# Optimization experiments

Measured on AMD Instinct MI355X. Metric: run time of the kernel, lower is better.

## Reference

```python
import jax, jax.numpy as jnp
import numpy as np
from jax import lax

D = 128      # d_model
NH = 8       # nhead
DIM = D // NH
B, H, W = 2, 160, 160
EPS_ATT = 1e-6


def setup_inputs() -> dict:
    key = jax.random.key(0)
    ks = iter(jax.random.split(key, 40))
    def n(*s):
        return jax.random.normal(next(ks), s, dtype=jnp.float32) * 0.05
    inp = {
        "x": jax.random.normal(next(ks), (B, D, H, W), jnp.float32),
        "source": jax.random.normal(next(ks), (B, D, H, W), jnp.float32),
        # q/k/v 1x1 conv (with bias)
        "wq": n(D, D), "bq": n(D),
        "wk": n(D, D), "bk": n(D),
        "wv": n(D, D), "bv": n(D),
        # multiscale aggregation (scale=5): depthwise 5x5 (no bias) + pointwise 1x1 (no bias)
        "dwq": n(D, 1, 5, 5), "pwq": n(D, D),
        "dwk": n(D, 1, 5, 5), "pwk": n(D, D),
        "dwv": n(D, 1, 5, 5), "pwv": n(D, D),
        # attention output projection: 2*d_model -> d_model, no bias
        "wproj": n(D, 2 * D),
        # merge 1x1 conv
        "wmerge": n(D, D), "bmerge": n(D),
        # conv ffn: d -> 2d -> d
        "wff1": n(2 * D, D), "bff1": n(2 * D),
        "wff2": n(D, 2 * D), "bff2": n(D),
        # layernorms over channel dim
        "ln1_w": 1.0 + n(D), "ln1_b": n(D),
        "ln2_w": 1.0 + n(D), "ln2_b": n(D),
    }
    return inp


def _pw(t, Wm, b=None):
    # 1x1 conv as channel matmul; t: [B,C,H,W], Wm: [O,C]
    y = jnp.einsum('bchw,oc->bohw', t, Wm)
    return y if b is None else y + b[None, :, None, None]


def _bn(t):
    # BatchNorm2d, training-mode batch stats, affine=False, eps=1e-5
    m = t.mean((0, 2, 3), keepdims=True)
    v = t.var((0, 2, 3), keepdims=True)
    return (t - m) * lax.rsqrt(v + 1e-5)


def _gelu(t):
    return jax.nn.gelu(t, approximate=False)


def _dw(t, Wk):
    # depthwise 5x5 conv, stride 1, SAME padding (== padding=2)
    return lax.conv_general_dilated(t, Wk, (1, 1), 'SAME',
                                    dimension_numbers=('NCHW', 'OIHW', 'NCHW'),
                                    feature_group_count=D)


def _ln(t, w, b):
    # LayerNorm over channel axis of NCHW tensor, eps=1e-5
    m = t.mean(1, keepdims=True)
    v = t.var(1, keepdims=True)
    return (t - m) * lax.rsqrt(v + 1e-5) * w[None, :, None, None] + b[None, :, None, None]


def reference(x, source, wq, bq, wk, bk, wv, bv, dwq, pwq, dwk, pwk, dwv, pwv,
              wproj, wmerge, bmerge, wff1, bff1, wff2, bff2,
              ln1_w, ln1_b, ln2_w, ln2_b):
    q = _gelu(_bn(_pw(x, wq, bq)))
    k = _gelu(_bn(_pw(source, wk, bk)))
    v = _gelu(_bn(_pw(source, wv, bv)))

    # multiscale aggregation: concat original with one scale-5 depthwise+pointwise branch
    qc = jnp.concatenate([q, _pw(_dw(q, dwq), pwq)], axis=1)
    kc = jnp.concatenate([k, _pw(_dw(k, dwk), pwk)], axis=1)
    vc = jnp.concatenate([v, _pw(_dw(v, dwv), pwv)], axis=1)

    qc = jax.nn.relu(qc)  # kernel feature map
    kc = jax.nn.relu(kc)

    b_, C2, h1, w1 = qc.shape           # C2 = 2*d_model
    h2, w2 = kc.shape[2], kc.shape[3]
    L1, L2 = h1 * w1, h2 * w2
    H2 = C2 // DIM                       # effective heads = 2*nhead

    qf = qc.reshape(b_, C2, L1).transpose(0, 2, 1).reshape(b_, L1, H2, DIM)
    kf = kc.reshape(b_, C2, L2).transpose(0, 2, 1).reshape(b_, L2, H2, DIM)
    vf = vc.reshape(b_, C2, L2).transpose(0, 2, 1).reshape(b_, L2, H2, DIM)

    vf = vf / L2
    kv = jnp.einsum('nshd,nshv->nhdv', kf, vf)                       # [b,H2,d,d]
    z = 1.0 / jnp.maximum(jnp.einsum('nlhd,nhd->nlh', qf, kf.sum(1) / L2), EPS_ATT)
    qv = jnp.einsum('nlhd,nhdv,nlh->nlhv', qf, kv, z)                # [b,L1,H2,d]

    out = qv.transpose(0, 2, 3, 1).reshape(b_, C2, h1, w1)
    msg = _pw(out, wproj)                                            # 2d -> d

    msg = _gelu(_bn(_pw(msg, wmerge, bmerge)))
    msg = x + msg
    msg = _ln(msg, ln1_w, ln1_b)

    ff = _gelu(_bn(_pw(msg, wff1, bff1)))
    ff = _gelu(_bn(_pw(ff, wff2, bff2)))
    return _ln(ff + msg, ln2_w, ln2_b)
```

## Files before the change

kernel.cpp:

```cpp
#include <hip/hip_runtime.h>
#include <math.h>

#define LL 25600
#define NTOTF 51200.f
#define NSH 8

using f16   = _Float16;
using f16x8 = __attribute__((ext_vector_type(8))) _Float16;
using f16x4 = __attribute__((ext_vector_type(4))) _Float16;
using f16x2 = __attribute__((ext_vector_type(2))) _Float16;
using f32x4 = __attribute__((ext_vector_type(4))) float;

__device__ __forceinline__ float gelu_f(float v) {
    const float u2 = v * (1.5957691216057308f + 0.0713548162726009f * v * v);
    const float e  = __expf(u2);
    return v * (1.f - 1.f / (e + 1.f));
}

__device__ __forceinline__ void stat_mr(const float* st, int C, int c,
                                        float& m, float& r) {
    float s1 = 0.f, s2 = 0.f;
#pragma unroll
    for (int sh = 0; sh < NSH; ++sh) {
        s1 += st[sh * 2 * C + c];
        s2 += st[sh * 2 * C + C + c];
    }
    m = s1 * (1.f / NTOTF);
    r = rsqrtf(s2 * (1.f / NTOTF) - m * m + 1e-5f);
}

template <int M, int K, int PP, int NSEG, bool IN32, bool LDG, bool TWOW,
          bool BIAS, bool STATS>
__global__ __launch_bounds__(512, 2) void gemm_kernel(
    const void* __restrict__ X1, const void* __restrict__ X2,
    const void* __restrict__ X3,
    const float* __restrict__ WA, const float* __restrict__ WB,
    const float* __restrict__ W2, const float* __restrict__ W3,
    const float* __restrict__ biasA, const float* __restrict__ biasB,
    const float* __restrict__ lstat,
    f16* __restrict__ Y1, f16* __restrict__ Y2, f16* __restrict__ Y3,
    float* __restrict__ ostat)
{
    constexpr int MR  = M / 128;
    constexpr int KS  = K / 32;
    constexpr int NR  = PP / 16;
    constexpr int PG  = PP / 8;
    constexpr int NCH = (K * PG) / 512;
    constexpr int NCHUNK = LL / PP;

    __shared__ f16 Xs[PP * K];

    const int tid  = threadIdx.x;
    const int lane = tid & 63;
    const int wv   = tid >> 6;
    const int lm16 = lane & 15, lg = lane >> 4;
    const int row0 = wv * (M / 8);

    int bx = blockIdx.x, seg = 0;
    if (NSEG > 1) { seg = bx / (2 * NCHUNK); bx -= seg * 2 * NCHUNK; }
    const int bb  = bx / NCHUNK;
    const int pp0 = (bx - bb * NCHUNK) * PP;

    const void*  Xp = (NSEG > 1) ? (seg == 0 ? X1 : (seg == 1 ? X2 : X3)) : X1;
    const float* Wp = (NSEG > 1) ? (seg == 0 ? WA : (seg == 1 ? W2 : W3)) : WA;
    f16*         Yp = (NSEG > 1) ? (seg == 0 ? Y1 : (seg == 1 ? Y2 : Y3)) : Y1;

    const int c0  = (tid / PG) * NCH;
    const int p0g = (tid % PG) * 8;

    f16x8 xin[NCH];
#pragma unroll
    for (int cc = 0; cc < NCH; ++cc) {
        const size_t roff = (size_t)(bb * K + c0 + cc) * LL + pp0 + p0g;
        if (IN32) {
            const float4 a  = *reinterpret_cast<const float4*>(
                                  reinterpret_cast<const float*>(Xp) + roff);
            const float4 b2 = *reinterpret_cast<const float4*>(
                                  reinterpret_cast<const float*>(Xp) + roff + 4);
            f16x8 v;
            v[0] = (f16)a.x;  v[1] = (f16)a.y;  v[2] = (f16)a.z;  v[3] = (f16)a.w;
            v[4] = (f16)b2.x; v[5] = (f16)b2.y; v[6] = (f16)b2.z; v[7] = (f16)b2.w;
            xin[cc] = v;
        } else {
            xin[cc] = *reinterpret_cast<const f16x8*>(
                          reinterpret_cast<const f16*>(Xp) + roff);
        }
    }

    f16x8 wfr[KS][MR];
#pragma unroll
    for (int k = 0; k < KS; ++k) {
        const int col = k * 32 + lg * 8;
#pragma unroll
        for (int mr = 0; mr < MR; ++mr) {
            const int row = row0 + mr * 16 + lm16;
            const float* wp = (TWOW && row >= 128)
                                  ? WB + (size_t)(row - 128) * K + col
                                  : Wp + (size_t)row * K + col;
            const float4 wa = *reinterpret_cast<const float4*>(wp);
            const float4 wb2 = *reinterpret_cast<const float4*>(wp + 4);
            f16x8 v;
            v[0] = (f16)wa.x; v[1] = (f16)wa.y; v[2] = (f16)wa.z; v[3] = (f16)wa.w;
            v[4] = (f16)wb2.x; v[5] = (f16)wb2.y; v[6] = (f16)wb2.z; v[7] = (f16)wb2.w;
            wfr[k][mr] = v;
        }
    }

    float bvv[MR], st1[MR], st2[MR];
#pragma unroll
    for (int mr = 0; mr < MR; ++mr) {
        const int o = row0 + mr * 16 + lm16;
        bvv[mr] = BIAS ? ((TWOW && o >= 128) ? biasB[o - 128] : biasA[o]) : 0.f;
        st1[mr] = 0.f; st2[mr] = 0.f;
    }

    if (LDG) {
#pragma unroll
        for (int cc = 0; cc < NCH; ++cc) {
            const int c = c0 + cc;
            float m, r;
            stat_mr(lstat, K, c, m, r);
#pragma unroll
            for (int j = 0; j < 8; ++j)
                xin[cc][j] = (f16)gelu_f(((float)xin[cc][j] - m) * r);
        }
    }

#pragma unroll
    for (int j = 0; j < 8; ++j) {
        const int pos = p0g + j;
        const int swz = ((pos & 7) ^ ((pos >> 3) & 7)) << 3;
        if constexpr (NCH == 8) {
            f16x8 v;
#pragma unroll
            for (int cc = 0; cc < 8; ++cc) v[cc] = xin[cc][j];
            *reinterpret_cast<f16x8*>(&Xs[(size_t)pos * K + (c0 ^ swz)]) = v;
        } else if constexpr (NCH == 4) {
            f16x4 v;
#pragma unroll
            for (int cc = 0; cc < 4; ++cc) v[cc] = xin[cc][j];
            *reinterpret_cast<f16x4*>(&Xs[(size_t)pos * K + (c0 ^ swz)]) = v;
        } else {
            f16x2 v;
#pragma unroll
            for (int cc = 0; cc < 2; ++cc) v[cc] = xin[cc][j];
            *reinterpret_cast<f16x2*>(&Xs[(size_t)pos * K + (c0 ^ swz)]) = v;
        }
    }
    __syncthreads();

    f32x4 acc[MR][NR];
#pragma unroll
    for (int mr = 0; mr < MR; ++mr)
#pragma unroll
        for (int nr = 0; nr < NR; ++nr)
            acc[mr][nr] = (f32x4){0.f, 0.f, 0.f, 0.f};

#pragma unroll
    for (int k = 0; k < KS; ++k) {
        const int kc = k * 32 + lg * 8;
        f16x8 xa[NR];
#pragma unroll
        for (int nr = 0; nr < NR; ++nr) {
            const int pos = nr * 16 + lm16;
            const int swz = ((pos & 7) ^ ((pos >> 3) & 7)) << 3;
            xa[nr] = *reinterpret_cast<const f16x8*>(
                &Xs[(size_t)pos * K + (kc ^ swz)]);
        }
#pragma unroll
        for (int mr = 0; mr < MR; ++mr)
#pragma unroll
            for (int nr = 0; nr < NR; ++nr)
                acc[mr][nr] = __builtin_amdgcn_mfma_f32_16x16x32_f16(
                    xa[nr], wfr[k][mr], acc[mr][nr], 0, 0, 0);
    }

#pragma unroll
    for (int mr = 0; mr < MR; ++mr) {
        const int o = row0 + mr * 16 + lm16;
        f16* yb = Yp + (size_t)(bb * M + o) * LL + pp0;
#pragma unroll
        for (int nr = 0; nr < NR; ++nr) {
            f16x4 o4;
#pragma unroll
            for (int r = 0; r < 4; ++r) {
                const float v = acc[mr][nr][r] + bvv[mr];
                o4[r] = (f16)v;
                if (STATS) { st1[mr] += v; st2[mr] += v * v; }
            }
            *reinterpret_cast<f16x4*>(yb + nr * 16 + lg * 4) = o4;
        }
    }

    if (STATS) {
        float* osb = ostat + (size_t)(blockIdx.x & (NSH - 1)) * 2 * M;
#pragma unroll
        for (int mr = 0; mr < MR; ++mr) {
            float s1 = st1[mr], s2 = st2[mr];
            s1 += __shfl_xor(s1, 16); s2 += __shfl_xor(s2, 16);
            s1 += __shfl_xor(s1, 32); s2 += __shfl_xor(s2, 32);
            if (lane < 16) {
                const int o = row0 + mr * 16 + lm16;
                atomicAdd(&osb[o], s1);
                atomicAdd(&osb[M + o], s2);
            }
        }
    }
}

__global__ __launch_bounds__(256) void act_kernel(
    const f16* __restrict__ qraw, const f16* __restrict__ kvraw,
    const float* __restrict__ sQ, const float* __restrict__ sKV,
    f16* __restrict__ actq, f16* __restrict__ actkv)
{
    const int idx = blockIdx.x * 256 + threadIdx.x;
    const f16* src; f16* dst; const float* st; int C, local;
    if (idx < 819200) { src = qraw;  dst = actq;  st = sQ;  C = 128; local = idx; }
    else              { src = kvraw; dst = actkv; st = sKV; C = 256; local = idx - 819200; }
    const int c = (local / 3200) % C;
    float m, r;
    stat_mr(st, C, c, m, r);
    const f16x8 v = *reinterpret_cast<const f16x8*>(src + (size_t)local * 8);
    f16x8 o;
#pragma unroll
    for (int j = 0; j < 8; ++j)
        o[j] = (f16)gelu_f(((float)v[j] - m) * r);
    *reinterpret_cast<f16x8*>(dst + (size_t)local * 8) = o;
}

__global__ __launch_bounds__(256) void dw5_kernel(
    const f16* __restrict__ actq, const f16* __restrict__ actkv,
    const float* __restrict__ dwq, const float* __restrict__ dwk,
    const float* __restrict__ dwv,
    f16* __restrict__ oq, f16* __restrict__ ok, f16* __restrict__ ov)
{
    __shared__ f16x2 pt[20][41];
    const int z = blockIdx.z;
    const int which = z >> 8;
    const int bc = z & 255;
    const int b = bc >> 7, c = bc & 127;

    const f16* src; const float* wdwp; f16* outp;
    if (which == 0)      { src = actq  + (size_t)(b * 128 + c) * LL;       wdwp = dwq + c * 25; outp = oq; }
    else if (which == 1) { src = actkv + (size_t)(b * 256 + c) * LL;       wdwp = dwk + c * 25; outp = ok; }
    else                 { src = actkv + (size_t)(b * 256 + 128 + c) * LL; wdwp = dwv + c * 25; outp = ov; }

    const int h0 = blockIdx.y * 32, w0 = blockIdx.x * 32;
    const int tid = threadIdx.x;

    f16x2 wp[25];
#pragma unroll
    for (int q = 0; q < 25; ++q) {
        const f16 wv16 = (f16)wdwp[q];
        wp[q][0] = wv16; wp[q][1] = wv16;
    }

    for (int idx = tid; idx < 720; idx += 256) {
        const int t  = idx / 36, cc = idx - t * 36;
        const int iw = w0 - 2 + cc;
        const int ih0 = h0 - 2 + t, ih1 = ih0 + 16;
        const int iwc  = min(max(iw, 0), 159);
        const int ihc0 = min(max(ih0, 0), 159);
        const int ihc1 = min(max(ih1, 0), 159);
        const bool okw = (iw >= 0) & (iw < 160);
        f16 lo = src[ihc0 * 160 + iwc];
        f16 hi = src[ihc1 * 160 + iwc];
        if (!(okw & (ih0 >= 0) & (ih0 < 160))) lo = (f16)0;
        if (!(okw & (ih1 >= 0) & (ih1 < 160))) hi = (f16)0;
        f16x2 pv; pv[0] = lo; pv[1] = hi;
        pt[t][cc] = pv;
    }
    __syncthreads();

    const int ylo = tid >> 4, xq = tid & 15, x0 = xq * 2;

    f16x2 a0; a0[0] = (f16)0; a0[1] = (f16)0;
    f16x2 a1 = a0;
#pragma unroll
    for (int u = 0; u < 5; ++u) {
        const f16x2* row = &pt[ylo + u][x0];
        const f16x2 r0 = row[0], r1 = row[1], r2 = row[2];
        const f16x2 r3 = row[3], r4 = row[4], r5 = row[5];
        a0 += wp[u*5+0] * r0;  a1 += wp[u*5+0] * r1;
        a0 += wp[u*5+1] * r1;  a1 += wp[u*5+1] * r2;
        a0 += wp[u*5+2] * r2;  a1 += wp[u*5+2] * r3;
        a0 += wp[u*5+3] * r3;  a1 += wp[u*5+3] * r4;
        a0 += wp[u*5+4] * r4;  a1 += wp[u*5+4] * r5;
    }

    f16* ob = outp + (size_t)(b * 128 + c) * LL + (size_t)(h0 + ylo) * 160 + (w0 + x0);
    f16x2 lo2; lo2[0] = a0[0]; lo2[1] = a1[0];
    f16x2 hi2; hi2[0] = a0[1]; hi2[1] = a1[1];
    *reinterpret_cast<f16x2*>(ob) = lo2;
    *reinterpret_cast<f16x2*>(ob + 16 * 160) = hi2;
}

__global__ __launch_bounds__(256) void att_reduce_kernel(
    const f16* __restrict__ ACT, const f16* __restrict__ K2,
    const f16* __restrict__ V2,
    float* __restrict__ kvout, float* __restrict__ ksum)
{
    __shared__ float kvred[4][256];

    const int bx = blockIdx.x;
    const int b = bx / 400;
    const int rem = bx - b * 400;
    const int h = rem / 25;
    const int chunk = rem - h * 25;
    const int tid = threadIdx.x;
    const int wv = tid >> 6, l = tid & 63;
    const int ch = l & 15, kg = l >> 4;
    const bool half1 = h < 8;

    const f16* kbase = half1 ? ACT + (size_t)(b * 256 + h * 16 + ch) * LL
                             : K2 + (size_t)(b * 128 + (h - 8) * 16 + ch) * LL;
    const f16* vbase = half1 ? ACT + (size_t)(b * 256 + 128 + h * 16 + ch) * LL
                             : V2 + (size_t)(b * 128 + (h - 8) * 16 + ch) * LL;

    f32x4 acc = (f32x4){0.f, 0.f, 0.f, 0.f};
    float ksacc = 0.f;
    const int base = chunk * 1024 + kg * 8;
#pragma unroll
    for (int it = 0; it < 8; ++it) {
        const int p = base + wv * 256 + it * 32;
        const f16x8 kf = *reinterpret_cast<const f16x8*>(kbase + p);
        const f16x8 vf = *reinterpret_cast<const f16x8*>(vbase + p);
        f16x8 ka;
#pragma unroll
        for (int j = 0; j < 8; ++j) {
            const f16 kv_ = kf[j];
            ka[j] = (kv_ > (f16)0) ? kv_ : (f16)0;
            ksacc += (float)ka[j];
        }
        acc = __builtin_amdgcn_mfma_f32_16x16x32_f16(ka, vf, acc, 0, 0, 0);
    }

    constexpr float s = 1.f / (float)LL;
#pragma unroll
    for (int r = 0; r < 4; ++r)
        kvred[wv][(kg * 4 + r) * 16 + ch] = acc[r];
    __syncthreads();
    {
        float t = kvred[0][tid] + kvred[1][tid] + kvred[2][tid] + kvred[3][tid];
        atomicAdd(&kvout[(size_t)(b * 16 + h) * 256 + tid], t * s);
    }

    float s1 = ksacc;
    s1 += __shfl_xor(s1, 16);
    s1 += __shfl_xor(s1, 32);
    if (l < 16) atomicAdd(&ksum[(size_t)(b * 16 + h) * 16 + ch], s1 * s);
}

__global__ __launch_bounds__(256) void att_apply_kernel(
    const f16* __restrict__ Q, const f16* __restrict__ Q2,
    const float* __restrict__ kvin, const float* __restrict__ ksumin,
    f16* __restrict__ att)
{
    __shared__ float kvs[256];
    __shared__ float kss[16];

    const int bx = blockIdx.x;
    const int b = bx / 1600;
    const int rem = bx - b * 1600;
    const int h = rem / 100;
    const int chunk = rem - h * 100;
    const int tid = threadIdx.x;
    const int p = chunk * 256 + tid;

    kvs[tid] = kvin[(size_t)b * 4096 + h * 256 + tid];
    if (tid < 16) kss[tid] = ksumin[(size_t)b * 256 + h * 16 + tid];
    __syncthreads();

    const f16* qb = (h < 8) ? Q + (size_t)(b * 128 + h * 16) * LL
                            : Q2 + (size_t)(b * 128 + (h - 8) * 16) * LL;
    float s[16];
#pragma unroll
    for (int d = 0; d < 16; ++d)
        s[d] = fmaxf((float)qb[(size_t)d * LL + p], 0.f);
    float denom = 0.f;
#pragma unroll
    for (int d = 0; d < 16; ++d) denom = fmaf(s[d], kss[d], denom);
    const float z = 1.f / fmaxf(denom, 1e-6f);

    f16* ob = att + (size_t)(b * 256 + h * 16) * LL + p;
#pragma unroll
    for (int e = 0; e < 16; ++e) {
        float acc = 0.f;
#pragma unroll
        for (int d = 0; d < 16; ++d)
            acc = fmaf(s[d], kvs[d * 16 + e], acc);
        ob[(size_t)e * LL] = (f16)(acc * z);
    }
}

template <bool RES32, bool OUT32>
__global__ __launch_bounds__(256) void fuse_ln_kernel(
    const f16* __restrict__ yconv, const void* __restrict__ residv,
    const float* __restrict__ stat,
    const float* __restrict__ lnw, const float* __restrict__ lnb,
    void* __restrict__ outv)
{
    __shared__ float t[128][65];
    __shared__ float mrs[128][2];
    __shared__ float red[4][64][2];
    __shared__ float mln[64], rln[64];

    const int bx = blockIdx.x;
    const int b = bx / 400, p0 = (bx - b * 400) * 64;
    const int tid = threadIdx.x;

    if (tid < 128) {
        float m, r;
        stat_mr(stat, 128, tid, m, r);
        mrs[tid][0] = m; mrs[tid][1] = r;
    }
    __syncthreads();

#pragma unroll
    for (int it = 0; it < 4; ++it) {
        const int chunk = it * 256 + tid;
        const int c  = chunk >> 3;
        const int pg = (chunk & 7) * 8;
        const size_t off = (size_t)(b * 128 + c) * LL + p0 + pg;
        const f16x8 yv = *reinterpret_cast<const f16x8*>(yconv + off);
        const float m = mrs[c][0], r = mrs[c][1];
        float rv[8];
        if (RES32) {
            const float* rp = reinterpret_cast<const float*>(residv) + off;
            const float4 ra = *reinterpret_cast<const float4*>(rp);
            const float4 rb = *reinterpret_cast<const float4*>(rp + 4);
            rv[0] = ra.x; rv[1] = ra.y; rv[2] = ra.z; rv[3] = ra.w;
            rv[4] = rb.x; rv[5] = rb.y; rv[6] = rb.z; rv[7] = rb.w;
        } else {
            const f16x8 rr = *reinterpret_cast<const f16x8*>(
                reinterpret_cast<const f16*>(residv) + off);
#pragma unroll
            for (int j = 0; j < 8; ++j) rv[j] = (float)rr[j];
        }
#pragma unroll
        for (int j = 0; j < 8; ++j)
            t[c][pg + j] = gelu_f(((float)yv[j] - m) * r) + rv[j];
    }
    __syncthreads();

    {
        const int i = tid & 63, q = tid >> 6;
        float ps = 0.f, pq = 0.f;
        for (int c = q * 32; c < q * 32 + 32; ++c) {
            const float v = t[c][i];
            ps += v; pq += v * v;
        }
        red[q][i][0] = ps; red[q][i][1] = pq;
    }
    __syncthreads();
    if (tid < 64) {
        float s1 = 0.f, s2 = 0.f;
#pragma unroll
        for (int q = 0; q < 4; ++q) { s1 += red[q][tid][0]; s2 += red[q][tid][1]; }
        const float m = s1 * (1.f / 128.f);
        const float var = s2 * (1.f / 128.f) - m * m;
        mln[tid] = m; rln[tid] = rsqrtf(var + 1e-5f);
    }
    __syncthreads();

#pragma unroll
    for (int it = 0; it < 4; ++it) {
        const int chunk = it * 256 + tid;
        const int c  = chunk >> 3;
        const int pg = (chunk & 7) * 8;
        const size_t off = (size_t)(b * 128 + c) * LL + p0 + pg;
        const float lw = lnw[c], lb = lnb[c];
        if (OUT32) {
            float4 oa, ob2;
            float* op = reinterpret_cast<float*>(outv) + off;
            oa.x = (t[c][pg+0] - mln[pg+0]) * rln[pg+0] * lw + lb;
            oa.y = (t[c][pg+1] - mln[pg+1]) * rln[pg+1] * lw + lb;
            oa.z = (t[c][pg+2] - mln[pg+2]) * rln[pg+2] * lw + lb;
            oa.w = (t[c][pg+3] - mln[pg+3]) * rln[pg+3] * lw + lb;
            ob2.x = (t[c][pg+4] - mln[pg+4]) * rln[pg+4] * lw + lb;
            ob2.y = (t[c][pg+5] - mln[pg+5]) * rln[pg+5] * lw + lb;
            ob2.z = (t[c][pg+6] - mln[pg+6]) * rln[pg+6] * lw + lb;
            ob2.w = (t[c][pg+7] - mln[pg+7]) * rln[pg+7] * lw + lb;
            *reinterpret_cast<float4*>(op) = oa;
            *reinterpret_cast<float4*>(op + 4) = ob2;
        } else {
            f16x8 o;
#pragma unroll
            for (int j = 0; j < 8; ++j)
                o[j] = (f16)((t[c][pg + j] - mln[pg + j]) * rln[pg + j] * lw + lb);
            *reinterpret_cast<f16x8*>(reinterpret_cast<f16*>(outv) + off) = o;
        }
    }
}

__global__ __launch_bounds__(256) void wcomb_kernel(
    const float* __restrict__ wmerge, const float* __restrict__ wproj,
    float* __restrict__ wc, float* __restrict__ zbase, int zcount)
{
    const int g = blockIdx.x * 256 + threadIdx.x;
    if (g < zcount) zbase[g] = 0.f;

    const int o = blockIdx.x;
    const int c2 = threadIdx.x;
    float acc = 0.f;
#pragma unroll 4
    for (int m = 0; m < 128; ++m)
        acc = fmaf(wmerge[o * 128 + m], wproj[m * 256 + c2], acc);
    wc[o * 256 + c2] = acc;
}

extern "C" void kernel_launch(void* const* d_in, const int* in_sizes, int n_in,
                              void* d_out, int out_size, void* d_ws, size_t ws_size,
                              hipStream_t stream)
{
    const float* x      = (const float*)d_in[0];
    const float* source = (const float*)d_in[1];
    const float* wq = (const float*)d_in[2];  const float* bq = (const float*)d_in[3];
    const float* wk = (const float*)d_in[4];  const float* bk = (const float*)d_in[5];
    const float* wvw = (const float*)d_in[6]; const float* bvb = (const float*)d_in[7];
    const float* dwq = (const float*)d_in[8];  const float* pwq = (const float*)d_in[9];
    const float* dwk = (const float*)d_in[10]; const float* pwk = (const float*)d_in[11];
    const float* dwv = (const float*)d_in[12]; const float* pwv = (const float*)d_in[13];
    const float* wproj  = (const float*)d_in[14];
    const float* wmerge = (const float*)d_in[15]; const float* bmerge = (const float*)d_in[16];
    const float* wff1 = (const float*)d_in[17]; const float* bff1 = (const float*)d_in[18];
    const float* wff2 = (const float*)d_in[19]; const float* bff2 = (const float*)d_in[20];
    const float* ln1w = (const float*)d_in[21]; const float* ln1b = (const float*)d_in[22];
    const float* ln2w = (const float*)d_in[23]; const float* ln2b = (const float*)d_in[24];

    const size_t UNIT  = (size_t)2 * 128 * LL;
    const size_t UNITB = UNIT * sizeof(f16);
    char* w = (char*)d_ws;
    f16* qraw  = (f16*)w; w += UNITB;
    f16* kvraw = (f16*)w; w += 2 * UNITB;
    f16* actq  = (f16*)w; w += UNITB;
    f16* actkv = (f16*)w; w += 2 * UNITB;
    f16* q2raw = (f16*)w; w += UNITB;
    f16* k2raw = (f16*)w; w += UNITB;
    f16* v2raw = (f16*)w; w += UNITB;
    f16* y2raw = (f16*)w; w += UNITB;
    f16* msg   = (f16*)w; w += UNITB;
    f16* ff1raw= (f16*)w; w += 2 * UNITB;
    f16* ff2raw= (f16*)w; w += UNITB;

    f16* dtq = qraw;
    f16* dtk = kvraw;
    f16* dtv = kvraw + UNIT;
    f16* att = actkv;

    float* zbase = (float*)w;
    float* kvred = zbase;
    float* ksum  = zbase + 8192;
    float* sQ    = zbase + 8704;
    float* sKV   = sQ + NSH * 256;
    float* sM    = sKV + NSH * 512;
    float* sF1   = sM + NSH * 256;
    float* sF2   = sF1 + NSH * 512;
    const int zcount = 8192 + 512 + NSH * (256 + 512 + 256 + 512 + 256);
    float* wcomb = zbase + zcount;

    wcomb_kernel<<<128, 256, 0, stream>>>(wmerge, wproj, wcomb, zbase, zcount);

    gemm_kernel<128,128,128,1,true,false,false,true,true><<<400, 512, 0, stream>>>(
        x, nullptr, nullptr, wq, nullptr, nullptr, nullptr, bq, nullptr, nullptr,
        qraw, nullptr, nullptr, sQ);
    gemm_kernel<256,128,64,1,true,false,true,true,true><<<800, 512, 0, stream>>>(
        source, nullptr, nullptr, wk, wvw, nullptr, nullptr, bk, bvb, nullptr,
        kvraw, nullptr, nullptr, sKV);

    act_kernel<<<9600, 256, 0, stream>>>(qraw, kvraw, sQ, sKV, actq, actkv);

    dim3 dwg(5, 5, 768);
    dw5_kernel<<<dwg, 256, 0, stream>>>(actq, actkv, dwq, dwk, dwv, dtq, dtk, dtv);
    gemm_kernel<128,128,128,3,false,false,false,false,false><<<1200, 512, 0, stream>>>(
        dtq, dtk, dtv, pwq, nullptr, pwk, pwv, nullptr, nullptr, nullptr,
        q2raw, k2raw, v2raw, nullptr);

    att_reduce_kernel<<<800, 256, 0, stream>>>(actkv, k2raw, v2raw, kvred, ksum);
    att_apply_kernel<<<3200, 256, 0, stream>>>(actq, q2raw, kvred, ksum, att);

    gemm_kernel<128,256,128,1,false,false,false,true,true><<<400, 512, 0, stream>>>(
        att, nullptr, nullptr, wcomb, nullptr, nullptr, nullptr, bmerge, nullptr,
        nullptr, y2raw, nullptr, nullptr, sM);

    fuse_ln_kernel<true,false><<<800, 256, 0, stream>>>(
        y2raw, x, sM, ln1w, ln1b, msg);

    gemm_kernel<256,128,64,1,false,false,false,true,true><<<800, 512, 0, stream>>>(
        msg, nullptr, nullptr, wff1, nullptr, nullptr, nullptr, bff1, nullptr,
        nullptr, ff1raw, nullptr, nullptr, sF1);
    gemm_kernel<128,256,128,1,false,true,false,true,true><<<400, 512, 0, stream>>>(
        ff1raw, nullptr, nullptr, wff2, nullptr, nullptr, nullptr, bff2, nullptr,
        sF1, ff2raw, nullptr, nullptr, sF2);

    fuse_ln_kernel<false,true><<<800, 256, 0, stream>>>(
        ff2raw, msg, sF2, ln2w, ln2b, (float*)d_out);
}
```

Before: 254.4 us.

## Add persistent double-buffered loop to M=256 GEMMs and halve their grids

Adds a LOOP template mode in which each block walks several pixel tiles in a grid-stride loop. It prefetches the next tile into registers while MFMAs run on the current one, using two LDS buffers. The two M=256 GEMMs (K/V projection and FFN1) now launch 400 blocks, each handling two tiles, so weight fragments are loaded once per block and the tile load overlaps compute. The cost is double the LDS, more register pressure and fewer blocks, which may lower occupancy and latency hiding.

After: 246.0 us. -3.3%, faster.

```diff
diff --git a/kernel.cpp b/kernel.cpp
--- a/kernel.cpp
+++ b/kernel.cpp
@@ -29,8 +29,8 @@
     r = rsqrtf(s2 * (1.f / NTOTF) - m * m + 1e-5f);
 }
 
-template <int M, int K, int PP, int NSEG, bool IN32, bool LDG, bool TWOW,
-          bool BIAS, bool STATS>
+template <int M, int K, int PP, int NSEG, bool LOOP, bool IN32, bool LDG,
+          bool TWOW, bool BIAS, bool STATS>
 __global__ __launch_bounds__(512, 2) void gemm_kernel(
     const void* __restrict__ X1, const void* __restrict__ X2,
     const void* __restrict__ X3,
@@ -47,8 +47,9 @@
     constexpr int PG  = PP / 8;
     constexpr int NCH = (K * PG) / 512;
     constexpr int NCHUNK = LL / PP;
-
-    __shared__ f16 Xs[PP * K];
+    constexpr int NBUF = LOOP ? 2 : 1;
+
+    __shared__ f16 Xs[NBUF * PP * K];
 
     const int tid  = threadIdx.x;
     const int lane = tid & 63;
@@ -58,8 +59,6 @@
 
     int bx = blockIdx.x, seg = 0;
     if (NSEG > 1) { seg = bx / (2 * NCHUNK); bx -= seg * 2 * NCHUNK; }
-    const int bb  = bx / NCHUNK;
-    const int pp0 = (bx - bb * NCHUNK) * PP;
 
     const void*  Xp = (NSEG > 1) ? (seg == 0 ? X1 : (seg == 1 ? X2 : X3)) : X1;
     const float* Wp = (NSEG > 1) ? (seg == 0 ? WA : (seg == 1 ? W2 : W3)) : WA;
@@ -69,23 +68,62 @@
     const int p0g = (tid % PG) * 8;
 
     f16x8 xin[NCH];
-#pragma unroll
-    for (int cc = 0; cc < NCH; ++cc) {
-        const size_t roff = (size_t)(bb * K + c0 + cc) * LL + pp0 + p0g;
-        if (IN32) {
-            const float4 a  = *reinterpret_cast<const float4*>(
-                                  reinterpret_cast<const float*>(Xp) + roff);
-            const float4 b2 = *reinterpret_cast<const float4*>(
-                                  reinterpret_cast<const float*>(Xp) + roff + 4);
-            f16x8 v;
-            v[0] = (f16)a.x;  v[1] = (f16)a.y;  v[2] = (f16)a.z;  v[3] = (f16)a.w;
-            v[4] = (f16)b2.x; v[5] = (f16)b2.y; v[6] = (f16)b2.z; v[7] = (f16)b2.w;
-            xin[cc] = v;
-        } else {
-            xin[cc] = *reinterpret_cast<const f16x8*>(
-                          reinterpret_cast<const f16*>(Xp) + roff);
-        }
-    }
+    auto load_regs = [&](int t) {
+        const int bb  = t / NCHUNK;
+        const int pp0 = (t - bb * NCHUNK) * PP;
+#pragma unroll
+        for (int cc = 0; cc < NCH; ++cc) {
+            const size_t roff = (size_t)(bb * K + c0 + cc) * LL + pp0 + p0g;
+            if (IN32) {
+                const float4 a  = *reinterpret_cast<const float4*>(
+                                      reinterpret_cast<const float*>(Xp) + roff);
+                const float4 b2 = *reinterpret_cast<const float4*>(
+                                      reinterpret_cast<const float*>(Xp) + roff + 4);
+                f16x8 v;
+                v[0] = (f16)a.x;  v[1] = (f16)a.y;  v[2] = (f16)a.z;  v[3] = (f16)a.w;
+                v[4] = (f16)b2.x; v[5] = (f16)b2.y; v[6] = (f16)b2.z; v[7] = (f16)b2.w;
+                xin[cc] = v;
+            } else {
+                xin[cc] = *reinterpret_cast<const f16x8*>(
+                              reinterpret_cast<const f16*>(Xp) + roff);
+            }
+        }
+    };
+    auto store_lds = [&](int buf) {
+        if (LDG) {
+#pragma unroll
+            for (int cc = 0; cc < NCH; ++cc) {
+                const int c = c0 + cc;
+                float m, r;
+                stat_mr(lstat, K, c, m, r);
+#pragma unroll
+                for (int j = 0; j < 8; ++j)
+                    xin[cc][j] = (f16)gelu_f(((float)xin[cc][j] - m) * r);
+            }
+        }
+#pragma unroll
+        for (int j = 0; j < 8; ++j) {
+            const int pos = p0g + j;
+            const int swz = ((pos & 7) ^ ((pos >> 3) & 7)) << 3;
+            f16* base = &Xs[(size_t)buf * PP * K + (size_t)pos * K];
+            if constexpr (NCH == 8) {
+                f16x8 v;
+#pragma unroll
+                for (int cc = 0; cc < 8; ++cc) v[cc] = xin[cc][j];
+                *reinterpret_cast<f16x8*>(base + (c0 ^ swz)) = v;
+            } else if constexpr (NCH == 4) {
+                f16x4 v;
+#pragma unroll
+                for (int cc = 0; cc < 4; ++cc) v[cc] = xin[cc][j];
+                *reinterpret_cast<f16x4*>(base + (c0 ^ swz)) = v;
+            } else {
+                f16x2 v;
+#pragma unroll
+                for (int cc = 0; cc < 2; ++cc) v[cc] = xin[cc][j];
+                *reinterpret_cast<f16x2*>(base + (c0 ^ swz)) = v;
+            }
+        }
+    };
 
     f16x8 wfr[KS][MR];
 #pragma unroll
@@ -114,82 +152,66 @@
         st1[mr] = 0.f; st2[mr] = 0.f;
     }
 
-    if (LDG) {
-#pragma unroll
-        for (int cc = 0; cc < NCH; ++cc) {
-            const int c = c0 + cc;
-            float m, r;
-            stat_mr(lstat, K, c, m, r);
-#pragma unroll
-            for (int j = 0; j < 8; ++j)
-                xin[cc][j] = (f16)gelu_f(((float)xin[cc][j] - m) * r);
-        }
-    }
-
-#pragma unroll
-    for (int j = 0; j < 8; ++j) {
-        const int pos = p0g + j;
-        const int swz = ((pos & 7) ^ ((pos >> 3) & 7)) << 3;
-        if constexpr (NCH == 8) {
-            f16x8 v;
-#pragma unroll
-            for (int cc = 0; cc < 8; ++cc) v[cc] = xin[cc][j];
-            *reinterpret_cast<f16x8*>(&Xs[(size_t)pos * K + (c0 ^ swz)]) = v;
-        } else if constexpr (NCH == 4) {
-            f16x4 v;
-#pragma unroll
-            for (int cc = 0; cc < 4; ++cc) v[cc] = xin[cc][j];
-            *reinterpret_cast<f16x4*>(&Xs[(size_t)pos * K + (c0 ^ swz)]) = v;
-        } else {
-            f16x2 v;
-#pragma unroll
-            for (int cc = 0; cc < 2; ++cc) v[cc] = xin[cc][j];
-            *reinterpret_cast<f16x2*>(&Xs[(size_t)pos * K + (c0 ^ swz)]) = v;
-        }
-    }
-    __syncthreads();
-
-    f32x4 acc[MR][NR];
-#pragma unroll
-    for (int mr = 0; mr < MR; ++mr)
-#pragma unroll
-        for (int nr = 0; nr < NR; ++nr)
-            acc[mr][nr] = (f32x4){0.f, 0.f, 0.f, 0.f};
-
-#pragma unroll
-    for (int k = 0; k < KS; ++k) {
-        const int kc = k * 32 + lg * 8;
-        f16x8 xa[NR];
-#pragma unroll
-        for (int nr = 0; nr < NR; ++nr) {
-            const int pos = nr * 16 + lm16;
-            const int swz = ((pos & 7) ^ ((pos >> 3) & 7)) << 3;
-            xa[nr] = *reinterpret_cast<const f16x8*>(
-                &Xs[(size_t)pos * K + (kc ^ swz)]);
-        }
+    int t = bx;
+    int cur = 0;
+    load_regs(t);
+    store_lds(0);
+    __syncthreads();
+
+    while (true) {
+        const int tn = t + gridDim.x;
+        const bool nxt = LOOP && (tn < (NSEG > 1 ? 2 * NCHUNK : 2 * NCHUNK));
+        if (nxt) load_regs(tn);
+
+        f32x4 acc[MR][NR];
 #pragma unroll
         for (int mr = 0; mr < MR; ++mr)
 #pragma unroll
             for (int nr = 0; nr < NR; ++nr)
-                acc[mr][nr] = __builtin_amdgcn_mfma_f32_16x16x32_f16(
-                    xa[nr], wfr[k][mr], acc[mr][nr], 0, 0, 0);
-    }
-
-#pragma unroll
-    for (int mr = 0; mr < MR; ++mr) {
-        const int o = row0 + mr * 16 + lm16;
-        f16* yb = Yp + (size_t)(bb * M + o) * LL + pp0;
-#pragma unroll
-        for (int nr = 0; nr < NR; ++nr) {
-            f16x4 o4;
-#pragma unroll
-            for (int r = 0; r < 4; ++r) {
-                const float v = acc[mr][nr][r] + bvv[mr];
-                o4[r] = (f16)v;
-                if (STATS) { st1[mr] += v; st2[mr] += v * v; }
+                acc[mr][nr] = (f32x4){0.f, 0.f, 0.f, 0.f};
+
+#pragma unroll
+        for (int k = 0; k < KS; ++k) {
+            const int kc = k * 32 + lg * 8;
+            f16x8 xa[NR];
+#pragma unroll
+            for (int nr = 0; nr < NR; ++nr) {
+                const int pos = nr * 16 + lm16;
+                const int swz = ((pos & 7) ^ ((pos >> 3) & 7)) << 3;
+                xa[nr] = *reinterpret_cast<const f16x8*>(
+                    &Xs[(size_t)cur * PP * K + (size_t)pos * K + (kc ^ swz)]);
             }
-            *reinterpret_cast<f16x4*>(yb + nr * 16 + lg * 4) = o4;
-        }
+#pragma unroll
+            for (int mr = 0; mr < MR; ++mr)
+#pragma unroll
+                for (int nr = 0; nr < NR; ++nr)
+                    acc[mr][nr] = __builtin_amdgcn_mfma_f32_16x16x32_f16(
+                        xa[nr], wfr[k][mr], acc[mr][nr], 0, 0, 0);
+        }
+
+        const int bb  = t / NCHUNK;
+        const int pp0 = (t - bb * NCHUNK) * PP;
+#pragma unroll
+        for (int mr = 0; mr < MR; ++mr) {
+            const int o = row0 + mr * 16 + lm16;
+            f16* yb = Yp + (size_t)(bb * M + o) * LL + pp0;
+#pragma unroll
+            for (int nr = 0; nr < NR; ++nr) {
+                f16x4 o4;
+#pragma unroll
+                for (int r = 0; r < 4; ++r) {
+                    const float v = acc[mr][nr][r] + bvv[mr];
+                    o4[r] = (f16)v;
+                    if (STATS) { st1[mr] += v; st2[mr] += v * v; }
+                }
+                *reinterpret_cast<f16x4*>(yb + nr * 16 + lg * 4) = o4;
+            }
+        }
+
+        if (!nxt) break;
+        store_lds(cur ^ 1);
+        __syncthreads();
+        cur ^= 1; t = tn;
     }
 
     if (STATS) {
@@ -561,10 +583,10 @@
 
     wcomb_kernel<<<128, 256, 0, stream>>>(wmerge, wproj, wcomb, zbase, zcount);
 
-    gemm_kernel<128,128,128,1,true,false,false,true,true><<<400, 512, 0, stream>>>(
+    gemm_kernel<128,128,128,1,false,true,false,false,true,true><<<400, 512, 0, stream>>>(
         x, nullptr, nullptr, wq, nullptr, nullptr, nullptr, bq, nullptr, nullptr,
         qraw, nullptr, nullptr, sQ);
-    gemm_kernel<256,128,64,1,true,false,true,true,true><<<800, 512, 0, stream>>>(
+    gemm_kernel<256,128,64,1,true,true,false,true,true,true><<<400, 512, 0, stream>>>(
         source, nullptr, nullptr, wk, wvw, nullptr, nullptr, bk, bvb, nullptr,
         kvraw, nullptr, nullptr, sKV);
 
@@ -572,24 +594,24 @@
 
     dim3 dwg(5, 5, 768);
     dw5_kernel<<<dwg, 256, 0, stream>>>(actq, actkv, dwq, dwk, dwv, dtq, dtk, dtv);
-    gemm_kernel<128,128,128,3,false,false,false,false,false><<<1200, 512, 0, stream>>>(
+    gemm_kernel<128,128,128,3,false,false,false,false,false,false><<<1200, 512, 0, stream>>>(
         dtq, dtk, dtv, pwq, nullptr, pwk, pwv, nullptr, nullptr, nullptr,
         q2raw, k2raw, v2raw, nullptr);
 
     att_reduce_kernel<<<800, 256, 0, stream>>>(actkv, k2raw, v2raw, kvred, ksum);
     att_apply_kernel<<<3200, 256, 0, stream>>>(actq, q2raw, kvred, ksum, att);
 
-    gemm_kernel<128,256,128,1,false,false,false,true,true><<<400, 512, 0, stream>>>(
+    gemm_kernel<128,256,128,1,false,false,false,false,true,true><<<400, 512, 0, stream>>>(
         att, nullptr, nullptr, wcomb, nullptr, nullptr, nullptr, bmerge, nullptr,
         nullptr, y2raw, nullptr, nullptr, sM);
 
     fuse_ln_kernel<true,false><<<800, 256, 0, stream>>>(
         y2raw, x, sM, ln1w, ln1b, msg);
 
-    gemm_kernel<256,128,64,1,false,false,false,true,true><<<800, 512, 0, stream>>>(
+    gemm_kernel<256,128,64,1,true,false,false,false,true,true><<<400, 512, 0, stream>>>(
         msg, nullptr, nullptr, wff1, nullptr, nullptr, nullptr, bff1, nullptr,
         nullptr, ff1raw, nullptr, nullptr, sF1);
-    gemm_kernel<128,256,128,1,false,true,false,true,true><<<400, 512, 0, stream>>>(
+    gemm_kernel<128,256,128,1,false,false,true,false,true,true><<<400, 512, 0, stream>>>(
         ff1raw, nullptr, nullptr, wff2, nullptr, nullptr, nullptr, bff2, nullptr,
         sF1, ff2raw, nullptr, nullptr, sF2);
 
```
